# Kernel tuning notes

Measured on AMD Instinct MI355X. Metric: run time of the kernel, lower is better.

## Reference

```python
import jax, jax.numpy as jnp
import numpy as np

MARGIN = 0.2
EPS = 1e-16


def setup_inputs() -> dict:
    key = jax.random.key(0)
    k1, k2, k3 = jax.random.split(key, 3)
    B, D, NCLASS = 512, 1024, 128
    labels = jax.random.randint(k1, (B,), 0, NCLASS, dtype=jnp.int64) if jax.config.jax_enable_x64 else jax.random.randint(k1, (B,), 0, NCLASS, dtype=jnp.int32)
    image_embeddings = jax.random.normal(k2, (B, D), dtype=jnp.float32)
    sentence_embeddings = jax.random.normal(k3, (B, D), dtype=jnp.float32)
    return {
        "labels": labels,
        "image_embeddings": image_embeddings,
        "sentence_embeddings": sentence_embeddings,
    }


def reference(labels, image_embeddings, sentence_embeddings):
    # pairwise "distance" (actually similarity) matrix [B, B]
    pairwise = jnp.matmul(image_embeddings, sentence_embeddings.T)
    # triplet tensor [a, p, n] = pairwise[a, p] - pairwise[a, n] + margin
    triplet = pairwise[:, :, None] - pairwise[:, None, :] + MARGIN
    # valid mask: labels[a] == labels[p] and labels[a] != labels[n]
    label_equal = labels[None, :] == labels[:, None]          # [B, B]
    mask = label_equal[:, :, None] & (~label_equal[:, None, :])  # [a, p, n]
    triplet = jnp.maximum(mask.astype(triplet.dtype) * triplet, 0.0)
    num_positive = jnp.sum(triplet > EPS).astype(triplet.dtype)
    return jnp.sum(triplet) / (num_positive + EPS)
```

## Files before the change

kernel.cpp:

```cpp
#include <hip/hip_runtime.h>

#define MARGIN 0.2f
#define EPSF   1e-16f

constexpr int BSZ  = 512;
constexpr int DIM  = 1024;
constexpr int RBLK = 128;
constexpr int PWSZ = BSZ * BSZ;

typedef __attribute__((ext_vector_type(8))) short    bf16x8;
typedef __attribute__((ext_vector_type(4))) unsigned uint4v;
typedef __attribute__((ext_vector_type(4))) float    f32x4;

__device__ __forceinline__ bf16x8 cvt8(float4 a, float4 b) {
    uint4v u;
    asm("v_cvt_pk_bf16_f32 %0, %1, %2" : "=v"(u[0]) : "v"(a.x), "v"(a.y));
    asm("v_cvt_pk_bf16_f32 %0, %1, %2" : "=v"(u[1]) : "v"(a.z), "v"(a.w));
    asm("v_cvt_pk_bf16_f32 %0, %1, %2" : "=v"(u[2]) : "v"(b.x), "v"(b.y));
    asm("v_cvt_pk_bf16_f32 %0, %1, %2" : "=v"(u[3]) : "v"(b.z), "v"(b.w));
    return __builtin_bit_cast(bf16x8, u);
}

__global__ void __launch_bounds__(256) mfma_gemm(const float* __restrict__ I,
                                                 const float* __restrict__ S,
                                                 float* __restrict__ pwp,
                                                 unsigned* __restrict__ ctr) {
    __shared__ f32x4 lds[4][16][64];

    const int tid  = threadIdx.x;
    const int lane = tid & 63;
    const int w    = tid >> 6;
    const int tid8 = ((blockIdx.x & 7) << 5) | (blockIdx.x >> 3);
    const int tile = tid8 >> 2;
    const int kq   = tid8 & 3;
    const int tr   = (tile >> 3) * 64;
    const int tc   = (tile & 7) * 64;
    const int r    = lane & 15;
    const int hi   = lane >> 4;
    const int kbase = kq * 256 + w * 64 + hi * 8;

    if (blockIdx.x == 0 && tid == 0) *ctr = 0u;

    const float* Ap[4];
    const float* Bp[4];
#pragma unroll
    for (int g = 0; g < 4; ++g) {
        Ap[g] = I + (size_t)(tr + g * 16 + r) * DIM + kbase;
        Bp[g] = S + (size_t)(tc + g * 16 + r) * DIM + kbase;
    }

    f32x4 acc[4][4];
#pragma unroll
    for (int g = 0; g < 4; ++g)
#pragma unroll
        for (int h = 0; h < 4; ++h)
            acc[g][h] = (f32x4){0.f, 0.f, 0.f, 0.f};

#pragma unroll
    for (int t = 0; t < 2; ++t) {
        bf16x8 fa[4], fb[4];
#pragma unroll
        for (int g = 0; g < 4; ++g)
            fa[g] = cvt8(*(const float4*)(Ap[g] + t * 32),
                         *(const float4*)(Ap[g] + t * 32 + 4));
#pragma unroll
        for (int h = 0; h < 4; ++h)
            fb[h] = cvt8(*(const float4*)(Bp[h] + t * 32),
                         *(const float4*)(Bp[h] + t * 32 + 4));
#pragma unroll
        for (int g = 0; g < 4; ++g)
#pragma unroll
            for (int h = 0; h < 4; ++h)
                acc[g][h] = __builtin_amdgcn_mfma_f32_16x16x32_bf16(
                                fa[g], fb[h], acc[g][h], 0, 0, 0);
    }

#pragma unroll
    for (int g = 0; g < 4; ++g)
#pragma unroll
        for (int h = 0; h < 4; ++h)
            lds[w][g * 4 + h][lane] = acc[g][h];
    __syncthreads();

    float* const plane = pwp + (size_t)kq * PWSZ;
#pragma unroll
    for (int i = 0; i < 4; ++i) {
        const int f = w * 4 + i;
        const int g = f >> 2, h = f & 3;
        f32x4 v = lds[0][f][lane];
        v += lds[1][f][lane];
        v += lds[2][f][lane];
        v += lds[3][f][lane];
        const int orow = tr + g * 16 + hi * 4;
        const int ocol = tc + h * 16 + r;
#pragma unroll
        for (int e = 0; e < 4; ++e)
            plane[(orow + e) * BSZ + ocol] = v[e];
    }
}

__global__ void __launch_bounds__(256) triplet_reduce(const float* __restrict__ pwp,
                                                      const int*   __restrict__ labels,
                                                      unsigned long long* __restrict__ part,
                                                      unsigned* __restrict__ ctr,
                                                      float* __restrict__ out) {
    __shared__ int   lab[BSZ];
    __shared__ float rows[4][BSZ];
    __shared__ float wsum_s[4];
    __shared__ int   wcnt_s[4];
    __shared__ unsigned is_last;

    const int tid  = threadIdx.x;
    const int lane = tid & 63;
    const int w    = tid >> 6;
    const int a0   = blockIdx.x * 4;

    if (tid < 128) ((int4*)lab)[tid] = ((const int4*)labels)[tid];
    {
        const float4* p0 = (const float4*)(pwp + 0 * (size_t)PWSZ + (size_t)a0 * BSZ);
        const float4* p1 = (const float4*)(pwp + 1 * (size_t)PWSZ + (size_t)a0 * BSZ);
        const float4* p2 = (const float4*)(pwp + 2 * (size_t)PWSZ + (size_t)a0 * BSZ);
        const float4* p3 = (const float4*)(pwp + 3 * (size_t)PWSZ + (size_t)a0 * BSZ);
#pragma unroll
        for (int j = 0; j < 2; ++j) {
            const int idx = tid + j * 256;
            float4 v = p0[idx];
            const float4 v1 = p1[idx], v2 = p2[idx], v3 = p3[idx];
            v.x += v1.x; v.y += v1.y; v.z += v1.z; v.w += v1.w;
            v.x += v2.x; v.y += v2.y; v.z += v2.z; v.w += v2.w;
            v.x += v3.x; v.y += v3.y; v.z += v3.z; v.w += v3.w;
            ((float4*)rows)[idx] = v;
        }
    }
    __syncthreads();

    const int la = lab[a0 + w];

    float vn[8];
    bool  ng[8];
#pragma unroll
    for (int j = 0; j < 8; ++j) {
        const int n = j * 64 + lane;
        vn[j] = rows[w][n];
        ng[j] = (lab[n] != la);
    }

    float sum = 0.f;
    int   cnt = 0;
    for (int p0 = 0; p0 < BSZ; p0 += 64) {
        unsigned long long m = __ballot(lab[p0 + lane] == la);
        while (m) {
            const int p = p0 + __ffsll((long long)m) - 1;
            m &= m - 1;
            const float pv = rows[w][p] + MARGIN;
#pragma unroll
            for (int j = 0; j < 8; ++j) {
                const float v = pv - vn[j];
                sum += ng[j] ? fmaxf(v, 0.f) : 0.f;
                cnt += (ng[j] && v > EPSF) ? 1 : 0;
            }
        }
    }

#pragma unroll
    for (int off = 32; off > 0; off >>= 1) {
        sum += __shfl_down(sum, off);
        cnt += __shfl_down(cnt, off);
    }
    if (lane == 0) { wsum_s[w] = sum; wcnt_s[w] = cnt; }
    __syncthreads();

    if (tid == 0) {
        const float s = wsum_s[0] + wsum_s[1] + wsum_s[2] + wsum_s[3];
        const float c = (float)(wcnt_s[0] + wcnt_s[1] + wcnt_s[2] + wcnt_s[3]);
        const float2 pk2 = make_float2(s, c);
        __hip_atomic_store(&part[blockIdx.x],
                           __builtin_bit_cast(unsigned long long, pk2),
                           __ATOMIC_RELAXED, __HIP_MEMORY_SCOPE_AGENT);
        asm volatile("s_waitcnt vmcnt(0)" ::: "memory");
        const unsigned old = __hip_atomic_fetch_add(ctr, 1u, __ATOMIC_RELAXED,
                                                    __HIP_MEMORY_SCOPE_AGENT);
        is_last = (old == (unsigned)(RBLK - 1)) ? 1u : 0u;
    }
    __syncthreads();

    if (is_last) {
        float s = 0.f, c = 0.f;
        if (tid < RBLK) {
            const unsigned long long v =
                __hip_atomic_load(&part[tid], __ATOMIC_RELAXED,
                                  __HIP_MEMORY_SCOPE_AGENT);
            const float2 f = __builtin_bit_cast(float2, v);
            s = f.x;
            c = f.y;
        }
#pragma unroll
        for (int off = 32; off > 0; off >>= 1) {
            s += __shfl_down(s, off);
            c += __shfl_down(c, off);
        }
        if (lane == 0) { wsum_s[w] = s; wcnt_s[w] = (int)c; }
        __syncthreads();
        if (tid == 0) {
            const float S_ = wsum_s[0] + wsum_s[1] + wsum_s[2] + wsum_s[3];
            const float C_ = (float)(wcnt_s[0] + wcnt_s[1] + wcnt_s[2] + wcnt_s[3]);
            out[0] = S_ / (C_ + EPSF);
        }
    }
}

extern "C" void kernel_launch(void* const* d_in, const int* in_sizes, int n_in,
                              void* d_out, int out_size, void* d_ws, size_t ws_size,
                              hipStream_t stream) {
    const int*   labels = (const int*)d_in[0];
    const float* img    = (const float*)d_in[1];
    const float* sen    = (const float*)d_in[2];
    float* out = (float*)d_out;

    unsigned*           ctr = (unsigned*)d_ws;
    float*              pwp = (float*)((char*)d_ws + 256);
    unsigned long long* part = (unsigned long long*)((char*)d_ws + 256 + 4 * (size_t)PWSZ * 4);

    mfma_gemm<<<256, 256, 0, stream>>>(img, sen, pwp, ctr);
    triplet_reduce<<<RBLK, 256, 0, stream>>>(pwp, labels, part, ctr, out);
}
```

Baseline: 17.82 us.

## Split GEMM K into eight partials and halve anchors per reduce block

The GEMM now splits K into 8 slices instead of 4, launching 512 blocks that each run a single MFMA step, and writes 8 partial planes. The reduce kernel launches 256 blocks that each handle 2 anchors, with two waves per anchor splitting the negatives. The aim is more parallelism and better latency hiding across both kernels. In exchange the partial-plane traffic doubles (8MB written and then read) and the final reduce sums 8 planes.

```diff
diff --git a/kernel.cpp b/kernel.cpp
--- a/kernel.cpp
+++ b/kernel.cpp
@@ -5,12 +5,14 @@
 
 constexpr int BSZ  = 512;
 constexpr int DIM  = 1024;
-constexpr int RBLK = 128;
+constexpr int NKP  = 8;
+constexpr int RBLK = 256;
 constexpr int PWSZ = BSZ * BSZ;
 
 typedef __attribute__((ext_vector_type(8))) short    bf16x8;
 typedef __attribute__((ext_vector_type(4))) unsigned uint4v;
 typedef __attribute__((ext_vector_type(4))) float    f32x4;
+using ull = unsigned long long;
 
 __device__ __forceinline__ bf16x8 cvt8(float4 a, float4 b) {
     uint4v u;
@@ -30,24 +32,16 @@
     const int tid  = threadIdx.x;
     const int lane = tid & 63;
     const int w    = tid >> 6;
-    const int tid8 = ((blockIdx.x & 7) << 5) | (blockIdx.x >> 3);
-    const int tile = tid8 >> 2;
-    const int kq   = tid8 & 3;
+    const int idx  = ((blockIdx.x & 7) << 6) | (blockIdx.x >> 3);
+    const int tile = idx >> 3;
+    const int kp   = idx & 7;
     const int tr   = (tile >> 3) * 64;
     const int tc   = (tile & 7) * 64;
     const int r    = lane & 15;
     const int hi   = lane >> 4;
-    const int kbase = kq * 256 + w * 64 + hi * 8;
+    const int kbase = kp * 128 + w * 32 + hi * 8;
 
     if (blockIdx.x == 0 && tid == 0) *ctr = 0u;
-
-    const float* Ap[4];
-    const float* Bp[4];
-#pragma unroll
-    for (int g = 0; g < 4; ++g) {
-        Ap[g] = I + (size_t)(tr + g * 16 + r) * DIM + kbase;
-        Bp[g] = S + (size_t)(tc + g * 16 + r) * DIM + kbase;
-    }
 
     f32x4 acc[4][4];
 #pragma unroll
@@ -56,24 +50,23 @@
         for (int h = 0; h < 4; ++h)
             acc[g][h] = (f32x4){0.f, 0.f, 0.f, 0.f};
 
-#pragma unroll
-    for (int t = 0; t < 2; ++t) {
-        bf16x8 fa[4], fb[4];
-#pragma unroll
-        for (int g = 0; g < 4; ++g)
-            fa[g] = cvt8(*(const float4*)(Ap[g] + t * 32),
-                         *(const float4*)(Ap[g] + t * 32 + 4));
+    bf16x8 fa[4], fb[4];
+#pragma unroll
+    for (int g = 0; g < 4; ++g) {
+        const float* Ap = I + (size_t)(tr + g * 16 + r) * DIM + kbase;
+        fa[g] = cvt8(*(const float4*)Ap, *(const float4*)(Ap + 4));
+    }
+#pragma unroll
+    for (int h = 0; h < 4; ++h) {
+        const float* Bp = S + (size_t)(tc + h * 16 + r) * DIM + kbase;
+        fb[h] = cvt8(*(const float4*)Bp, *(const float4*)(Bp + 4));
+    }
+#pragma unroll
+    for (int g = 0; g < 4; ++g)
 #pragma unroll
         for (int h = 0; h < 4; ++h)
-            fb[h] = cvt8(*(const float4*)(Bp[h] + t * 32),
-                         *(const float4*)(Bp[h] + t * 32 + 4));
-#pragma unroll
-        for (int g = 0; g < 4; ++g)
-#pragma unroll
-            for (int h = 0; h < 4; ++h)
-                acc[g][h] = __builtin_amdgcn_mfma_f32_16x16x32_bf16(
-                                fa[g], fb[h], acc[g][h], 0, 0, 0);
-    }
+            acc[g][h] = __builtin_amdgcn_mfma_f32_16x16x32_bf16(
+                            fa[g], fb[h], acc[g][h], 0, 0, 0);
 
 #pragma unroll
     for (int g = 0; g < 4; ++g)
@@ -82,7 +75,7 @@
             lds[w][g * 4 + h][lane] = acc[g][h];
     __syncthreads();
 
-    float* const plane = pwp + (size_t)kq * PWSZ;
+    float* const plane = pwp + (size_t)kp * PWSZ;
 #pragma unroll
     for (int i = 0; i < 4; ++i) {
         const int f = w * 4 + i;
@@ -101,11 +94,11 @@
 
 __global__ void __launch_bounds__(256) triplet_reduce(const float* __restrict__ pwp,
                                                       const int*   __restrict__ labels,
-                                                      unsigned long long* __restrict__ part,
+                                                      ull* __restrict__ part,
                                                       unsigned* __restrict__ ctr,
                                                       float* __restrict__ out) {
     __shared__ int   lab[BSZ];
-    __shared__ float rows[4][BSZ];
+    __shared__ float rows[2][BSZ];
     __shared__ float wsum_s[4];
     __shared__ int   wcnt_s[4];
     __shared__ unsigned is_last;
@@ -113,35 +106,31 @@
     const int tid  = threadIdx.x;
     const int lane = tid & 63;
     const int w    = tid >> 6;
-    const int a0   = blockIdx.x * 4;
+    const int a0   = blockIdx.x * 2;
 
     if (tid < 128) ((int4*)lab)[tid] = ((const int4*)labels)[tid];
     {
-        const float4* p0 = (const float4*)(pwp + 0 * (size_t)PWSZ + (size_t)a0 * BSZ);
-        const float4* p1 = (const float4*)(pwp + 1 * (size_t)PWSZ + (size_t)a0 * BSZ);
-        const float4* p2 = (const float4*)(pwp + 2 * (size_t)PWSZ + (size_t)a0 * BSZ);
-        const float4* p3 = (const float4*)(pwp + 3 * (size_t)PWSZ + (size_t)a0 * BSZ);
-#pragma unroll
-        for (int j = 0; j < 2; ++j) {
-            const int idx = tid + j * 256;
-            float4 v = p0[idx];
-            const float4 v1 = p1[idx], v2 = p2[idx], v3 = p3[idx];
-            v.x += v1.x; v.y += v1.y; v.z += v1.z; v.w += v1.w;
-            v.x += v2.x; v.y += v2.y; v.z += v2.z; v.w += v2.w;
-            v.x += v3.x; v.y += v3.y; v.z += v3.z; v.w += v3.w;
-            ((float4*)rows)[idx] = v;
-        }
-    }
-    __syncthreads();
-
-    const int la = lab[a0 + w];
-
-    float vn[8];
-    bool  ng[8];
-#pragma unroll
-    for (int j = 0; j < 8; ++j) {
-        const int n = j * 64 + lane;
-        vn[j] = rows[w][n];
+        const float4* p0 = (const float4*)(pwp + (size_t)a0 * BSZ);
+        float4 v = p0[tid];
+#pragma unroll
+        for (int p = 1; p < NKP; ++p) {
+            const float4 u = ((const float4*)(pwp + (size_t)p * PWSZ + (size_t)a0 * BSZ))[tid];
+            v.x += u.x; v.y += u.y; v.z += u.z; v.w += u.w;
+        }
+        ((float4*)rows)[tid] = v;
+    }
+    __syncthreads();
+
+    const int aw = w >> 1;
+    const int nb = (w & 1) * 256;
+    const int la = lab[a0 + aw];
+
+    float vn[4];
+    bool  ng[4];
+#pragma unroll
+    for (int j = 0; j < 4; ++j) {
+        const int n = nb + j * 64 + lane;
+        vn[j] = rows[aw][n];
         ng[j] = (lab[n] != la);
     }
 
@@ -152,9 +141,9 @@
         while (m) {
             const int p = p0 + __ffsll((long long)m) - 1;
             m &= m - 1;
-            const float pv = rows[w][p] + MARGIN;
-#pragma unroll
-            for (int j = 0; j < 8; ++j) {
+            const float pv = rows[aw][p] + MARGIN;
+#pragma unroll
+            for (int j = 0; j < 4; ++j) {
                 const float v = pv - vn[j];
                 sum += ng[j] ? fmaxf(v, 0.f) : 0.f;
                 cnt += (ng[j] && v > EPSF) ? 1 : 0;
@@ -174,8 +163,7 @@
         const float s = wsum_s[0] + wsum_s[1] + wsum_s[2] + wsum_s[3];
         const float c = (float)(wcnt_s[0] + wcnt_s[1] + wcnt_s[2] + wcnt_s[3]);
         const float2 pk2 = make_float2(s, c);
-        __hip_atomic_store(&part[blockIdx.x],
-                           __builtin_bit_cast(unsigned long long, pk2),
+        __hip_atomic_store(&part[blockIdx.x], __builtin_bit_cast(ull, pk2),
                            __ATOMIC_RELAXED, __HIP_MEMORY_SCOPE_AGENT);
         asm volatile("s_waitcnt vmcnt(0)" ::: "memory");
         const unsigned old = __hip_atomic_fetch_add(ctr, 1u, __ATOMIC_RELAXED,
@@ -185,15 +173,10 @@
     __syncthreads();
 
     if (is_last) {
-        float s = 0.f, c = 0.f;
-        if (tid < RBLK) {
-            const unsigned long long v =
-                __hip_atomic_load(&part[tid], __ATOMIC_RELAXED,
-                                  __HIP_MEMORY_SCOPE_AGENT);
-            const float2 f = __builtin_bit_cast(float2, v);
-            s = f.x;
-            c = f.y;
-        }
+        const ull v = __hip_atomic_load(&part[tid], __ATOMIC_RELAXED,
+                                        __HIP_MEMORY_SCOPE_AGENT);
+        const float2 f = __builtin_bit_cast(float2, v);
+        float s = f.x, c = f.y;
 #pragma unroll
         for (int off = 32; off > 0; off >>= 1) {
             s += __shfl_down(s, off);
@@ -217,10 +200,10 @@
     const float* sen    = (const float*)d_in[2];
     float* out = (float*)d_out;
 
-    unsigned*           ctr = (unsigned*)d_ws;
-    float*              pwp = (float*)((char*)d_ws + 256);
-    unsigned long long* part = (unsigned long long*)((char*)d_ws + 256 + 4 * (size_t)PWSZ * 4);
-
-    mfma_gemm<<<256, 256, 0, stream>>>(img, sen, pwp, ctr);
+    unsigned* ctr  = (unsigned*)d_ws;
+    float*    pwp  = (float*)((char*)d_ws + 256);
+    ull*      part = (ull*)((char*)d_ws + 256 + (size_t)NKP * PWSZ * 4);
+
+    mfma_gemm<<<512, 256, 0, stream>>>(img, sen, pwp, ctr);
     triplet_reduce<<<RBLK, 256, 0, stream>>>(pwp, labels, part, ctr, out);
 }
```

New measurement: 21.31 us. +19.6%, slower.
